# Optimization experiments

Hardware: AMD Instinct MI355X
Metric: run time of the kernel (lower is better)

## Reference

```python
import jax, jax.numpy as jnp
import numpy as np

B, S = 65536, 128          # batch of tasks, support set size
MAX_CLASSES = 10
STATS_DIM = MAX_CLASSES + 4  # hist + [n_nonzero, entropy, subset_size, hist_max]
TOKEN_DIM = 256


def setup_inputs() -> dict:
    key = jax.random.key(0)
    k1, k2, k3, k4, k5 = jax.random.split(key, 5)
    y_support = jax.random.randint(k1, (B, S), 0, MAX_CLASSES, dtype=jnp.int32)
    # MLP params: Linear(14, D) -> GELU -> Linear(D, D)
    w1 = jax.random.normal(k2, (STATS_DIM, TOKEN_DIM), jnp.float32) / np.sqrt(STATS_DIM)
    b1 = jax.random.normal(k3, (TOKEN_DIM,), jnp.float32) * 0.01
    w2 = jax.random.normal(k4, (TOKEN_DIM, TOKEN_DIM), jnp.float32) / np.sqrt(TOKEN_DIM)
    b2 = jax.random.normal(k5, (TOKEN_DIM,), jnp.float32) * 0.01
    return {"y_support": y_support, "w1": w1, "b1": b1, "w2": w2, "b2": b2}


def reference(y_support, w1, b1, w2, b2):
    b, s = y_support.shape
    # Batched bincount via scatter-add: hist[i, c] = #{j : y_support[i, j] == c}
    rows = jnp.arange(b, dtype=jnp.int32)[:, None]              # [B, 1]
    hist = jnp.zeros((b, MAX_CLASSES), jnp.float32).at[rows, y_support].add(1.0)
    total = jnp.maximum(hist.sum(axis=-1, keepdims=True), 1.0)  # clamp_min(1.0)
    p = hist / total                                            # [B, C]
    entropy = -(p * jnp.log(p + 1e-6)).sum(axis=-1)             # [B]
    n_nonzero = (p > 0).sum(axis=-1).astype(jnp.float32)        # [B]
    stats = jnp.concatenate([
        p,
        n_nonzero[:, None],
        entropy[:, None],
        jnp.full((b, 1), float(s), jnp.float32),
        p.max(axis=-1, keepdims=True),
    ], axis=1)                                                  # [B, C+4]
    h = jax.nn.gelu(stats @ w1 + b1, approximate=False)         # exact GELU like nn.GELU
    return h @ w2 + b2                                          # [B, TOKEN_DIM]
```

## Files before the change

### kernel.cpp

```cpp
#include <hip/hip_runtime.h>
#include <stdint.h>


#define SSUP 128
#define DD   256

typedef __attribute__((ext_vector_type(8)))  short bf16x8;
typedef __attribute__((ext_vector_type(16))) float f32x16;

__device__ __forceinline__ unsigned f2bf_u(float f) {
    union { float f; unsigned u; } v; v.f = f;
    return (v.u + 0x7FFFu + ((v.u >> 16) & 1u)) >> 16;
}
__device__ __forceinline__ unsigned pk2(float a, float b) {
    return f2bf_u(a) | (f2bf_u(b) << 16);
}

__device__ __forceinline__ float gelu_f(float x) {
    float z = 0.7978845608028654f * x * (1.0f + 0.044715f * x * x);
    float e = __expf(-2.0f * z);
    float th = 2.0f / (1.0f + e) - 1.0f;
    return 0.5f * x * (1.0f + th);
}

__global__ void prep_kernel(const float* __restrict__ w1,
                            const float* __restrict__ w2,
                            unsigned short* __restrict__ w1f,
                            unsigned short* __restrict__ w2f) {
    int tid = blockIdx.x * 256 + threadIdx.x;
    if (tid < 8192) {
        int l  = tid & 63;
        int nt = (tid >> 6) & 7;
        int s  = tid >> 9;
        int n  = nt * 32 + (l & 31);
        int k0 = s * 16 + (l >> 5) * 8;
        unsigned pk[4];
        #pragma unroll
        for (int h = 0; h < 4; ++h)
            pk[h] = pk2(w2[(size_t)(k0 + 2*h) * DD + n],
                        w2[(size_t)(k0 + 2*h + 1) * DD + n]);
        *(uint4*)&w2f[(size_t)tid * 8] = make_uint4(pk[0], pk[1], pk[2], pk[3]);
    } else if (tid < 8704) {
        int idx = tid - 8192;
        int l   = idx & 63;
        int nt  = idx >> 6;
        int n   = nt * 32 + (l & 31);
        int kk0 = (l >> 5) * 8;
        unsigned pk[4];
        #pragma unroll
        for (int h = 0; h < 4; ++h) {
            int ka = kk0 + 2*h, kb = kk0 + 2*h + 1;
            float fa = (ka < 14) ? w1[(size_t)ka * DD + n] : 0.0f;
            float fb = (kb < 14) ? w1[(size_t)kb * DD + n] : 0.0f;
            pk[h] = pk2(fa, fb);
        }
        *(uint4*)&w1f[(size_t)idx * 8] = make_uint4(pk[0], pk[1], pk[2], pk[3]);
    }
}

__global__ __launch_bounds__(512, 8)
void encoder_kernel(const int* __restrict__ y,
                    const float* __restrict__ b1,
                    const float* __restrict__ b2,
                    const unsigned short* __restrict__ w1f,
                    const unsigned short* __restrict__ w2f,
                    float* __restrict__ out) {
    __shared__ __align__(16) unsigned short stats_a[64][16];
    __shared__ __align__(16) unsigned short h_lds[64][264];

    const int tid = threadIdx.x;
    const int r0 = blockIdx.x * 64;

    const int rl = tid >> 3;
    const int q  = tid & 7;
    const int4* yp = (const int4*)(y + (size_t)(r0 + rl) * SSUP);
    unsigned long long pkc = 0ull;
    #pragma unroll
    for (int i = 0; i < 4; ++i) {
        int4 v = yp[i * 8 + q];
        pkc += 1ull << (6 * v.x);
        pkc += 1ull << (6 * v.y);
        pkc += 1ull << (6 * v.z);
        pkc += 1ull << (6 * v.w);
    }
    float p[10]; float ent = 0.f, pmax = 0.f, nnz = 0.f;
    #pragma unroll
    for (int c = 0; c < 10; ++c) {
        int cc = (int)((pkc >> (6 * c)) & 63ull);
        cc += __shfl_xor(cc, 1);
        cc += __shfl_xor(cc, 2);
        cc += __shfl_xor(cc, 4);
        float pc = (float)cc * 0.0078125f;
        p[c] = pc;
        nnz += (cc > 0) ? 1.0f : 0.0f;
        ent -= pc * __logf(pc + 1e-6f);
        pmax = fmaxf(pmax, pc);
    }
    if (q < 2) {
        unsigned a0, a1, a2, a3;
        if (q == 0) { a0 = pk2(p[0], p[1]); a1 = pk2(p[2], p[3]);
                      a2 = pk2(p[4], p[5]); a3 = pk2(p[6], p[7]); }
        else        { a0 = pk2(p[8], p[9]); a1 = pk2(nnz, ent);
                      a2 = pk2(128.0f, pmax); a3 = 0u; }
        *(uint4*)&stats_a[rl][q * 8] = make_uint4(a0, a1, a2, a3);
    }
    __syncthreads();

    const int lane = tid & 63;
    const int wid  = tid >> 6;
    const int wm   = wid & 1;
    const int wn   = wid >> 1;
    const int l31  = lane & 31;
    const int lh   = lane >> 5;
    const int m    = 32 * wm + l31;

    bf16x8 sfrag = *(const bf16x8*)&stats_a[m][lh * 8];
    #pragma unroll
    for (int t = 0; t < 2; ++t) {
        const int nt = wn * 2 + t;
        bf16x8 wfrag = *(const bf16x8*)&w1f[(size_t)(nt * 64 + lane) * 8];
        f32x16 c;
        #pragma unroll
        for (int g = 0; g < 4; ++g) {
            float4 bv = *(const float4*)&b1[nt * 32 + 8 * g + 4 * lh];
            c[4*g+0] = bv.x; c[4*g+1] = bv.y; c[4*g+2] = bv.z; c[4*g+3] = bv.w;
        }
        c = __builtin_amdgcn_mfma_f32_32x32x16_bf16(wfrag, sfrag, c, 0, 0, 0);
        #pragma unroll
        for (int g = 0; g < 4; ++g) {
            unsigned u0 = pk2(gelu_f(c[4*g+0]), gelu_f(c[4*g+1]));
            unsigned u1 = pk2(gelu_f(c[4*g+2]), gelu_f(c[4*g+3]));
            *(uint2*)&h_lds[m][nt * 32 + 8 * g + 4 * lh] = make_uint2(u0, u1);
        }
    }
    __syncthreads();

    f32x16 acc[2];
    #pragma unroll
    for (int u = 0; u < 2; ++u) {
        const int nt = wn * 2 + u;
        #pragma unroll
        for (int g = 0; g < 4; ++g) {
            float4 bv = *(const float4*)&b2[nt * 32 + 8 * g + 4 * lh];
            acc[u][4*g+0] = bv.x; acc[u][4*g+1] = bv.y;
            acc[u][4*g+2] = bv.z; acc[u][4*g+3] = bv.w;
        }
    }
    #pragma unroll
    for (int s = 0; s < 16; ++s) {
        bf16x8 hfrag = *(const bf16x8*)&h_lds[m][s * 16 + lh * 8];
        #pragma unroll
        for (int u = 0; u < 2; ++u) {
            const int nt = wn * 2 + u;
            bf16x8 wfrag = *(const bf16x8*)
                &w2f[(size_t)((s * 8 + nt) * 64 + lane) * 8];
            acc[u] = __builtin_amdgcn_mfma_f32_32x32x16_bf16(wfrag, hfrag, acc[u], 0, 0, 0);
        }
    }
    #pragma unroll
    for (int u = 0; u < 2; ++u) {
        const int nt = wn * 2 + u;
        #pragma unroll
        for (int g = 0; g < 4; ++g) {
            float4 o;
            o.x = acc[u][4*g+0]; o.y = acc[u][4*g+1];
            o.z = acc[u][4*g+2]; o.w = acc[u][4*g+3];
            *(float4*)&out[(size_t)(r0 + m) * DD + nt * 32 + 8 * g + 4 * lh] = o;
        }
    }
}

extern "C" void kernel_launch(void* const* d_in, const int* in_sizes, int n_in,
                              void* d_out, int out_size, void* d_ws, size_t ws_size,
                              hipStream_t stream) {
    const int*   y  = (const int*)d_in[0];
    const float* w1 = (const float*)d_in[1];
    const float* b1 = (const float*)d_in[2];
    const float* w2 = (const float*)d_in[3];
    const float* b2 = (const float*)d_in[4];
    float* out = (float*)d_out;

    unsigned short* w2f = (unsigned short*)d_ws;
    unsigned short* w1f = w2f + 65536;

    prep_kernel<<<34, 256, 0, stream>>>(w1, w2, w1f, w2f);

    const int nrows = in_sizes[0] / SSUP;
    encoder_kernel<<<nrows / 64, 512, 0, stream>>>(y, b1, b2, w1f, w2f, out);
}
```

Measured before the change: 120.7 us.

## Keep each wave's 32 rows fully in registers, dropping LDS and barriers

Each wave now owns 32 rows end to end. It computes histograms with two lanes per row and builds the stats fragment with shuffles, then keeps the GELU hidden activations in 64 registers exchanged via cross-half shuffles instead of staging them through LDS with block barriers. Blocks shrink to 256 threads covering 128 rows, and each wave does all 8 output tiles. The GELU tanh form is also simplified algebraically to x*rcp(1+exp(-2z)). This removes LDS traffic and syncthreads but raises register pressure and makes each wave stream the full w2 weights from cache.

```diff
diff --git a/kernel.cpp b/kernel.cpp
--- a/kernel.cpp
+++ b/kernel.cpp
@@ -17,10 +17,10 @@
 }
 
 __device__ __forceinline__ float gelu_f(float x) {
-    float z = 0.7978845608028654f * x * (1.0f + 0.044715f * x * x);
-    float e = __expf(-2.0f * z);
-    float th = 2.0f / (1.0f + e) - 1.0f;
-    return 0.5f * x * (1.0f + th);
+    float t = x * x;
+    float u = __builtin_fmaf(t, 0.035677408136f, 0.7978845608028654f);
+    float e = __expf(x * u * -2.0f);
+    return x * __builtin_amdgcn_rcpf(1.0f + e);
 }
 
 __global__ void prep_kernel(const float* __restrict__ w1,
@@ -58,114 +58,118 @@
     }
 }
 
-__global__ __launch_bounds__(512, 8)
+__global__ __launch_bounds__(256, 4)
 void encoder_kernel(const int* __restrict__ y,
                     const float* __restrict__ b1,
                     const float* __restrict__ b2,
                     const unsigned short* __restrict__ w1f,
                     const unsigned short* __restrict__ w2f,
                     float* __restrict__ out) {
-    __shared__ __align__(16) unsigned short stats_a[64][16];
-    __shared__ __align__(16) unsigned short h_lds[64][264];
+    const int tid  = threadIdx.x;
+    const int lane = tid & 63;
+    const int wid  = tid >> 6;
+    const int l31  = lane & 31;
+    const int lh   = lane >> 5;
+    const int rbase = blockIdx.x * 128 + wid * 32;
 
-    const int tid = threadIdx.x;
-    const int r0 = blockIdx.x * 64;
-
-    const int rl = tid >> 3;
-    const int q  = tid & 7;
-    const int4* yp = (const int4*)(y + (size_t)(r0 + rl) * SSUP);
-    unsigned long long pkc = 0ull;
+    const int hrow = lane >> 1;
+    const int hq   = lane & 1;
+    const int4* yp = (const int4*)(y + (size_t)(rbase + hrow) * SSUP);
+    unsigned long long pka = 0ull, pkb = 0ull;
     #pragma unroll
-    for (int i = 0; i < 4; ++i) {
-        int4 v = yp[i * 8 + q];
-        pkc += 1ull << (6 * v.x);
-        pkc += 1ull << (6 * v.y);
-        pkc += 1ull << (6 * v.z);
-        pkc += 1ull << (6 * v.w);
+    for (int i = 0; i < 8; ++i) {
+        int4 v = yp[2 * i + hq];
+        pka += 1ull << (6 * v.x);
+        pka += 1ull << (6 * v.y);
+        pka += 1ull << (6 * v.z);
+        pka += 1ull << (6 * v.w);
+    }
+    #pragma unroll
+    for (int i = 8; i < 16; ++i) {
+        int4 v = yp[2 * i + hq];
+        pkb += 1ull << (6 * v.x);
+        pkb += 1ull << (6 * v.y);
+        pkb += 1ull << (6 * v.z);
+        pkb += 1ull << (6 * v.w);
     }
     float p[10]; float ent = 0.f, pmax = 0.f, nnz = 0.f;
     #pragma unroll
     for (int c = 0; c < 10; ++c) {
-        int cc = (int)((pkc >> (6 * c)) & 63ull);
+        int cc = (int)((pka >> (6 * c)) & 63ull) + (int)((pkb >> (6 * c)) & 63ull);
         cc += __shfl_xor(cc, 1);
-        cc += __shfl_xor(cc, 2);
-        cc += __shfl_xor(cc, 4);
         float pc = (float)cc * 0.0078125f;
         p[c] = pc;
         nnz += (cc > 0) ? 1.0f : 0.0f;
         ent -= pc * __logf(pc + 1e-6f);
         pmax = fmaxf(pmax, pc);
     }
-    if (q < 2) {
-        unsigned a0, a1, a2, a3;
-        if (q == 0) { a0 = pk2(p[0], p[1]); a1 = pk2(p[2], p[3]);
-                      a2 = pk2(p[4], p[5]); a3 = pk2(p[6], p[7]); }
-        else        { a0 = pk2(p[8], p[9]); a1 = pk2(nnz, ent);
-                      a2 = pk2(128.0f, pmax); a3 = 0u; }
-        *(uint4*)&stats_a[rl][q * 8] = make_uint4(a0, a1, a2, a3);
-    }
-    __syncthreads();
+    unsigned sp0 = hq ? pk2(p[8], p[9])     : pk2(p[0], p[1]);
+    unsigned sp1 = hq ? pk2(nnz, ent)       : pk2(p[2], p[3]);
+    unsigned sp2 = hq ? pk2(128.0f, pmax)   : pk2(p[4], p[5]);
+    unsigned sp3 = hq ? 0u                  : pk2(p[6], p[7]);
+    const int src = 2 * l31 + lh;
+    union { unsigned u[4]; bf16x8 v; } sf;
+    sf.u[0] = __shfl((int)sp0, src);
+    sf.u[1] = __shfl((int)sp1, src);
+    sf.u[2] = __shfl((int)sp2, src);
+    sf.u[3] = __shfl((int)sp3, src);
+    const bf16x8 sfrag = sf.v;
 
-    const int lane = tid & 63;
-    const int wid  = tid >> 6;
-    const int wm   = wid & 1;
-    const int wn   = wid >> 1;
-    const int l31  = lane & 31;
-    const int lh   = lane >> 5;
-    const int m    = 32 * wm + l31;
-
-    bf16x8 sfrag = *(const bf16x8*)&stats_a[m][lh * 8];
+    unsigned hreg[64];
     #pragma unroll
-    for (int t = 0; t < 2; ++t) {
-        const int nt = wn * 2 + t;
-        bf16x8 wfrag = *(const bf16x8*)&w1f[(size_t)(nt * 64 + lane) * 8];
+    for (int nt = 0; nt < 8; ++nt) {
+        union { unsigned u[4]; bf16x8 v; } wf;
+        *(uint4*)wf.u = *(const uint4*)&w1f[(size_t)(nt * 64 + lane) * 8];
         f32x16 c;
         #pragma unroll
         for (int g = 0; g < 4; ++g) {
             float4 bv = *(const float4*)&b1[nt * 32 + 8 * g + 4 * lh];
             c[4*g+0] = bv.x; c[4*g+1] = bv.y; c[4*g+2] = bv.z; c[4*g+3] = bv.w;
         }
-        c = __builtin_amdgcn_mfma_f32_32x32x16_bf16(wfrag, sfrag, c, 0, 0, 0);
+        c = __builtin_amdgcn_mfma_f32_32x32x16_bf16(wf.v, sfrag, c, 0, 0, 0);
+        unsigned own[8], rcv[8];
         #pragma unroll
         for (int g = 0; g < 4; ++g) {
-            unsigned u0 = pk2(gelu_f(c[4*g+0]), gelu_f(c[4*g+1]));
-            unsigned u1 = pk2(gelu_f(c[4*g+2]), gelu_f(c[4*g+3]));
-            *(uint2*)&h_lds[m][nt * 32 + 8 * g + 4 * lh] = make_uint2(u0, u1);
+            own[2*g+0] = pk2(gelu_f(c[4*g+0]), gelu_f(c[4*g+1]));
+            own[2*g+1] = pk2(gelu_f(c[4*g+2]), gelu_f(c[4*g+3]));
+        }
+        #pragma unroll
+        for (int j = 0; j < 8; ++j) rcv[j] = (unsigned)__shfl_xor((int)own[j], 32);
+        #pragma unroll
+        for (int t = 0; t < 2; ++t) {
+            const int b = nt * 8 + t * 4;
+            hreg[b+0] = lh ? rcv[4*t+2] : own[4*t+0];
+            hreg[b+1] = lh ? rcv[4*t+3] : own[4*t+1];
+            hreg[b+2] = lh ? own[4*t+2] : rcv[4*t+0];
+            hreg[b+3] = lh ? own[4*t+3] : rcv[4*t+1];
         }
     }
-    __syncthreads();
 
-    f32x16 acc[2];
     #pragma unroll
-    for (int u = 0; u < 2; ++u) {
-        const int nt = wn * 2 + u;
+    for (int nt = 0; nt < 8; ++nt) {
+        f32x16 acc;
         #pragma unroll
         for (int g = 0; g < 4; ++g) {
             float4 bv = *(const float4*)&b2[nt * 32 + 8 * g + 4 * lh];
-            acc[u][4*g+0] = bv.x; acc[u][4*g+1] = bv.y;
-            acc[u][4*g+2] = bv.z; acc[u][4*g+3] = bv.w;
+            acc[4*g+0] = bv.x; acc[4*g+1] = bv.y;
+            acc[4*g+2] = bv.z; acc[4*g+3] = bv.w;
         }
-    }
-    #pragma unroll
-    for (int s = 0; s < 16; ++s) {
-        bf16x8 hfrag = *(const bf16x8*)&h_lds[m][s * 16 + lh * 8];
         #pragma unroll
-        for (int u = 0; u < 2; ++u) {
-            const int nt = wn * 2 + u;
-            bf16x8 wfrag = *(const bf16x8*)
-                &w2f[(size_t)((s * 8 + nt) * 64 + lane) * 8];
-            acc[u] = __builtin_amdgcn_mfma_f32_32x32x16_bf16(wfrag, hfrag, acc[u], 0, 0, 0);
+        for (int s = 0; s < 16; ++s) {
+            union { unsigned u[4]; bf16x8 v; } wf;
+            *(uint4*)wf.u = *(const uint4*)&w2f[(size_t)((s * 8 + nt) * 64 + lane) * 8];
+            union { unsigned u[4]; bf16x8 v; } bf;
+            const int b = (s >> 1) * 8 + (s & 1) * 4;
+            bf.u[0] = hreg[b+0]; bf.u[1] = hreg[b+1];
+            bf.u[2] = hreg[b+2]; bf.u[3] = hreg[b+3];
+            acc = __builtin_amdgcn_mfma_f32_32x32x16_bf16(wf.v, bf.v, acc, 0, 0, 0);
         }
-    }
-    #pragma unroll
-    for (int u = 0; u < 2; ++u) {
-        const int nt = wn * 2 + u;
         #pragma unroll
         for (int g = 0; g < 4; ++g) {
             float4 o;
-            o.x = acc[u][4*g+0]; o.y = acc[u][4*g+1];
-            o.z = acc[u][4*g+2]; o.w = acc[u][4*g+3];
-            *(float4*)&out[(size_t)(r0 + m) * DD + nt * 32 + 8 * g + 4 * lh] = o;
+            o.x = acc[4*g+0]; o.y = acc[4*g+1];
+            o.z = acc[4*g+2]; o.w = acc[4*g+3];
+            *(float4*)&out[(size_t)(rbase + l31) * DD + nt * 32 + 8 * g + 4 * lh] = o;
         }
     }
 }
@@ -186,5 +190,5 @@
     prep_kernel<<<34, 256, 0, stream>>>(w1, w2, w1f, w2f);
 
     const int nrows = in_sizes[0] / SSUP;
-    encoder_kernel<<<nrows / 64, 512, 0, stream>>>(y, b1, b2, w1f, w2f, out);
+    encoder_kernel<<<nrows / 128, 256, 0, stream>>>(y, b1, b2, w1f, w2f, out);
 }
```

Result: slower. 146.3 us (+21.2%).
